# Optimization experiments

Hardware: AMD Instinct MI355X
Metric: run time of the kernel (lower is better)

Reference implementation:

```python
import jax, jax.numpy as jnp
import numpy as np


def ternarize_weight(w):
    # abs-mean threshold quantization to {-am, 0, +am}
    abs_mean = jnp.maximum(jnp.abs(w).mean(), 1e-5)
    thr = 0.7 * abs_mean
    q = jnp.where(w > thr, 1.0, jnp.where(w < -thr, -1.0, 0.0))
    # STE: forward value is q*abs_mean, grad flows to w as identity
    return w + jax.lax.stop_gradient(q * abs_mean - w)


def rotate_half(x):
    x1, x2 = jnp.split(x, 2, axis=-1)
    return jnp.concatenate([-x2, x1], axis=-1)


def setup_inputs() -> dict:
    key = jax.random.key(0)
    k1, k2, k3, k4, k5 = jax.random.split(key, 5)
    B, T, C, H = 2, 2048, 1024, 16
    D = C // H
    x = jax.random.normal(k1, (B, T, C), dtype=jnp.float32)
    cos = jax.random.uniform(k2, (1, 1, T, D), dtype=jnp.float32)
    sin = jax.random.uniform(k3, (1, 1, T, D), dtype=jnp.float32)
    w_qkv = jax.random.normal(k4, (3 * C, C), dtype=jnp.float32) / np.sqrt(C)
    w_proj = jax.random.normal(k5, (C, C), dtype=jnp.float32) / np.sqrt(C)
    return {"x": x, "cos": cos, "sin": sin, "w_qkv": w_qkv, "w_proj": w_proj}


def reference(x, cos, sin, w_qkv, w_proj):
    B, T, C = x.shape
    H = 16
    D = C // H
    wq = ternarize_weight(w_qkv)
    wp = ternarize_weight(w_proj)
    qkv = x @ wq.T  # [B,T,3C]
    q, k, v = jnp.split(qkv, 3, axis=-1)
    # [B,T,C] -> [B,H,T,D]
    q = q.reshape(B, T, H, D).transpose(0, 2, 1, 3)
    k = k.reshape(B, T, H, D).transpose(0, 2, 1, 3)
    v = v.reshape(B, T, H, D).transpose(0, 2, 1, 3)
    # RoPE
    q = q * cos + rotate_half(q) * sin
    k = k * cos + rotate_half(k) * sin
    # causal SDPA
    scale = 1.0 / np.sqrt(D)
    scores = jnp.einsum("bhqd,bhkd->bhqk", q, k) * scale
    causal = jnp.tril(jnp.ones((T, T), dtype=bool))
    scores = jnp.where(causal, scores, jnp.finfo(scores.dtype).min)
    attn = jax.nn.softmax(scores, axis=-1)
    y = jnp.einsum("bhqk,bhkd->bhqd", attn, v)  # [B,H,T,D]
    y = y.transpose(0, 2, 1, 3).reshape(B, T, C)
    return y @ wp.T
```

## Files before the change

### kernel.cpp

```cpp
#include <hip/hip_runtime.h>
#include <hip/hip_bf16.h>

#define B_ 2
#define T_ 2048
#define C_ 1024
#define H_ 16
#define D_ 64
#define M_ 4096
#define N3C 3072

using short8  = __attribute__((ext_vector_type(8))) short;
using floatx4 = __attribute__((ext_vector_type(4))) float;
typedef unsigned int u32;

__device__ __forceinline__ unsigned short f2b(float f) {
  __hip_bfloat16 h = __float2bfloat16(f);
  return *reinterpret_cast<unsigned short*>(&h);
}
__device__ __forceinline__ u32 pk2(float a, float b) {
  float2 t; t.x = a; t.y = b;
  __hip_bfloat162 p = __float22bfloat162_rn(t);
  return *reinterpret_cast<u32*>(&p);
}

#if __has_builtin(__builtin_amdgcn_exp2f)
__device__ __forceinline__ float ex2(float x) { return __builtin_amdgcn_exp2f(x); }
#else
__device__ __forceinline__ float ex2(float x) { return exp2f(x); }
#endif

__device__ __forceinline__ void gll16(const void* g, void* l) {
  __builtin_amdgcn_global_load_lds((const __attribute__((address_space(1))) u32*)g,
                                   (__attribute__((address_space(3))) u32*)l, 16, 0, 0);
}

#define SYNCV(N) do {                                                   \
    asm volatile("s_waitcnt vmcnt(" #N ")" ::: "memory");               \
    __builtin_amdgcn_s_barrier();                                       \
    asm volatile("" ::: "memory");                                      \
  } while (0)

__device__ __forceinline__ short8 xpnd(uint2 p) {
  u32 a = p.x, b = p.y;
  u32 d0 = ((a << 8) & 0x0000FF00u) | ((a << 16) & 0xFF000000u);
  u32 d1 = ((a >> 8) & 0x0000FF00u) | (a & 0xFF000000u);
  u32 d2 = ((b << 8) & 0x0000FF00u) | ((b << 16) & 0xFF000000u);
  u32 d3 = ((b >> 8) & 0x0000FF00u) | (b & 0xFF000000u);
  union { u32 d[4]; short8 s; } r;
  r.d[0] = d0; r.d[1] = d1; r.d[2] = d2; r.d[3] = d3;
  return r.s;
}


__global__ void abs_sum2(const float* __restrict__ wq, const float* __restrict__ wp,
                         double* __restrict__ sums) {
  __shared__ double red[4];
  const float* w = blockIdx.y ? wp : wq;
  const int n4 = blockIdx.y ? (C_ * C_ / 4) : (3 * C_ * C_ / 4);
  int stride = gridDim.x * blockDim.x;
  double s = 0.0;
  for (int i = blockIdx.x * blockDim.x + threadIdx.x; i < n4; i += stride) {
    float4 v = ((const float4*)w)[i];
    s += (double)fabsf(v.x) + (double)fabsf(v.y) + (double)fabsf(v.z) + (double)fabsf(v.w);
  }
  #pragma unroll
  for (int off = 32; off > 0; off >>= 1)
    s += __shfl_down(s, off, 64);
  if ((threadIdx.x & 63) == 0) red[threadIdx.x >> 6] = s;
  __syncthreads();
  if (threadIdx.x == 0) atomicAdd(sums + blockIdx.y, (red[0] + red[1]) + (red[2] + red[3]));
}

__global__ void tern_cvt(const float* __restrict__ wq, const float* __restrict__ wp,
                         const float* __restrict__ x,
                         unsigned char* __restrict__ oq, unsigned char* __restrict__ op,
                         unsigned short* __restrict__ xb,
                         const double* __restrict__ sums, float* __restrict__ ams) {
  const int NQ = 3 * C_ * C_;
  const int NP = C_ * C_;
  int i = blockIdx.x * blockDim.x + threadIdx.x;
  float am0 = fmaxf((float)(sums[0] * (1.0 / NQ)), 1e-5f);
  float am1 = fmaxf((float)(sums[1] * (1.0 / NP)), 1e-5f);
  if (i == 0) { ams[0] = am0; ams[1] = am1; }
  if (i < NQ) {
    float thr = 0.7f * am0, v = wq[i];
    oq[i] = (v > thr) ? 0x40u : ((v < -thr) ? 0xC0u : 0u);
  } else if (i < NQ + NP) {
    int j = i - NQ;
    float thr = 0.7f * am1, v = wp[j];
    op[j] = (v > thr) ? 0x40u : ((v < -thr) ? 0xC0u : 0u);
  } else {
    int j = i - NQ - NP;
    float4 v = ((const float4*)x)[j];
    ushort4 o; o.x = f2b(v.x); o.y = f2b(v.y); o.z = f2b(v.z); o.w = f2b(v.w);
    ((ushort4*)xb)[j] = o;
  }
}


__global__ __launch_bounds__(256) void gemm_qkv(const unsigned short* __restrict__ A,
                                                const unsigned char* __restrict__ W8,
                                                const float* __restrict__ scale_ptr,
                                                const float* __restrict__ cosp,
                                                const float* __restrict__ sinp,
                                                unsigned short* __restrict__ Qb,
                                                unsigned short* __restrict__ Kb,
                                                unsigned short* __restrict__ Vtb) {
  const int K = C_;
  __shared__ __attribute__((aligned(16))) unsigned short As[3][128 * 32];
  __shared__ __attribute__((aligned(16))) unsigned char  Ws[3][192 * 32];
  const int tid = threadIdx.x, lane = tid & 63, wv = tid >> 6;
  const int m = lane & 15, g = lane >> 4;
  const int m0 = blockIdx.y * 128, n0 = blockIdx.x * 192;
  const int wm = (wv >> 1) * 64, wn = wv & 1;
  const bool wlow = (wv < 2);

  const int srow16 = lane >> 2;
  const int skoff = (lane & 3) * 8;
  const unsigned short* ga0 = A + (size_t)(m0 + wv * 32 + srow16) * K + skoff;
  const unsigned short* ga1 = A + (size_t)(m0 + wv * 32 + 16 + srow16) * K + skoff;
  const unsigned char* gw0 = W8 + (size_t)(n0 + wv * 32 + (lane >> 1)) * K + (lane & 1) * 16;
  const unsigned char* gw1 = W8 + (size_t)(n0 + 128 + wv * 32 + (lane >> 1)) * K + (lane & 1) * 16;
  const int oA0 = (wv * 32) * 32;
  const int oA1 = (wv * 32 + 16) * 32;
  const int oW0 = (wv * 32) * 32;
  const int oW1 = ((128 + wv * 32)) * 32;

  floatx4 acc[4][6] = {};

#define QSTAGE(T) do {                                                    \
    gll16(ga0, &As[T][oA0]); gll16(ga1, &As[T][oA1]);                     \
    gll16(gw0, &Ws[T][oW0]);                                              \
    if (wlow) gll16(gw1, &Ws[T][oW1]);                                    \
    ga0 += 32; ga1 += 32; gw0 += 32; gw1 += 32;                           \
  } while (0)

#define QSYNC() do {                                                      \
    if (wlow) asm volatile("s_waitcnt vmcnt(4)" ::: "memory");            \
    else      asm volatile("s_waitcnt vmcnt(3)" ::: "memory");            \
    __builtin_amdgcn_s_barrier();                                         \
    asm volatile("" ::: "memory");                                        \
  } while (0)

#define QCOMP(T) do {                                                     \
    short8 af[4], wf[6];                                                  \
    _Pragma("unroll")                                                     \
    for (int r = 0; r < 4; r++)                                           \
      af[r] = *(const short8*)&As[T][(wm + r * 16 + m) * 32 + g * 8];     \
    _Pragma("unroll")                                                     \
    for (int j = 0; j < 6; j++)                                           \
      wf[j] = xpnd(*(const uint2*)&Ws[T][((2 * j + wn) * 16 + m) * 32 + g * 8]); \
    _Pragma("unroll")                                                     \
    for (int r = 0; r < 4; r++)                                           \
      _Pragma("unroll")                                                   \
      for (int j = 0; j < 6; j++)                                         \
        acc[r][j] = __builtin_amdgcn_mfma_f32_16x16x32_bf16(af[r], wf[j], acc[r][j], 0, 0, 0); \
  } while (0)

  QSTAGE(0);
  QSTAGE(1);
  QSYNC();
  for (int tt = 0; tt < 10; ++tt) {
    QSTAGE(2); QCOMP(0); QSYNC();
    QSTAGE(0); QCOMP(1); QSYNC();
    QSTAGE(1); QCOMP(2); QSYNC();
  }
  QCOMP(0); SYNCV(0);
  QCOMP(1);
#undef QSTAGE
#undef QSYNC
#undef QCOMP

  const float am = *scale_ptr;
  const float amh = am * 0.5f;
  #pragma unroll
  for (int j = 0; j < 6; j++) {
    const int colb = n0 + (2 * j + wn) * 16;
    const int sect = colb >> 10;
    const int h = (colb >> 6) & 15;
    const int pb = colb & 63;
    const int p = pb + m;
    if (sect < 2) {
      unsigned short* dst = sect ? Kb : Qb;
      const float sc = sect ? amh : amh * 0.18033688011112042f;
      const bool hi = (pb & 32) != 0;
      #pragma unroll
      for (int r = 0; r < 4; r++)
        #pragma unroll
        for (int i = 0; i < 4; i++) {
          int row = m0 + wm + r * 16 + g * 4 + i;
          int t = row & (T_ - 1), b = row >> 11;
          float cv = cosp[t * 64 + p], sv = sinp[t * 64 + p];
          float a = acc[r][j][i], pt = acc[r][j ^ 1][i];
          float val = hi ? (a * cv + pt * sv) : (a * cv - pt * sv);
          dst[((size_t)(b * H_ + h) * T_ + t) * 64 + p] = f2b(val * sc);
        }
    } else {
      #pragma unroll
      for (int r = 0; r < 4; r++)
        #pragma unroll
        for (int i = 0; i < 4; i++) {
          int row = m0 + wm + r * 16 + g * 4 + i;
          int t = row & (T_ - 1), b = row >> 11;
          size_t hbase = (size_t)(b * H_ + h) * 64 * T_;
          Vtb[hbase + (size_t)p * T_ + t] = f2b(acc[r][j][i] * amh);
        }
    }
  }
}


__global__ __launch_bounds__(256) void gemm_proj(const unsigned short* __restrict__ A,
                                                 const unsigned char* __restrict__ W8,
                                                 const float* __restrict__ scale_ptr,
                                                 float* __restrict__ Cout) {
  const int K = C_, N = C_;
  __shared__ __attribute__((aligned(16))) unsigned short As[3][128 * 32];
  __shared__ __attribute__((aligned(16))) unsigned char  Ws[3][128 * 32];
  const int tid = threadIdx.x, lane = tid & 63, wv = tid >> 6;
  const int m = lane & 15, g = lane >> 4;
  const int m0 = blockIdx.y * 128, n0 = blockIdx.x * 128;
  const int wm = (wv >> 1) * 64, wn = (wv & 1) * 64;

  const int srow16 = lane >> 2;
  const int skoff = (lane & 3) * 8;
  const unsigned short* ga0 = A + (size_t)(m0 + wv * 32 + srow16) * K + skoff;
  const unsigned short* ga1 = A + (size_t)(m0 + wv * 32 + 16 + srow16) * K + skoff;
  const unsigned char* gw0 = W8 + (size_t)(n0 + wv * 32 + (lane >> 1)) * K + (lane & 1) * 16;
  const int oA0 = (wv * 32) * 32;
  const int oA1 = (wv * 32 + 16) * 32;
  const int oW0 = (wv * 32) * 32;

  floatx4 acc[4][4] = {};

#define PSTAGE(T) do {                                                    \
    gll16(ga0, &As[T][oA0]); gll16(ga1, &As[T][oA1]);                     \
    gll16(gw0, &Ws[T][oW0]);                                              \
    ga0 += 32; ga1 += 32; gw0 += 32;                                      \
  } while (0)

#define PCOMP(T) do {                                                     \
    short8 af[4], wf[4];                                                  \
    _Pragma("unroll")                                                     \
    for (int r = 0; r < 4; r++)                                           \
      af[r] = *(const short8*)&As[T][(wm + r * 16 + m) * 32 + g * 8];     \
    _Pragma("unroll")                                                     \
    for (int c = 0; c < 4; c++)                                           \
      wf[c] = xpnd(*(const uint2*)&Ws[T][(wn + c * 16 + m) * 32 + g * 8]); \
    _Pragma("unroll")                                                     \
    for (int r = 0; r < 4; r++)                                           \
      _Pragma("unroll")                                                   \
      for (int c = 0; c < 4; c++)                                         \
        acc[r][c] = __builtin_amdgcn_mfma_f32_16x16x32_bf16(af[r], wf[c], acc[r][c], 0, 0, 0); \
  } while (0)

  PSTAGE(0);
  PSTAGE(1);
  SYNCV(3);
  for (int tt = 0; tt < 10; ++tt) {
    PSTAGE(2); PCOMP(0); SYNCV(3);
    PSTAGE(0); PCOMP(1); SYNCV(3);
    PSTAGE(1); PCOMP(2); SYNCV(3);
  }
  PCOMP(0); SYNCV(0);
  PCOMP(1);
#undef PSTAGE
#undef PCOMP

  const float scale = *scale_ptr * 0.5f;
  #pragma unroll
  for (int r = 0; r < 4; r++)
    #pragma unroll
    for (int c = 0; c < 4; c++)
      #pragma unroll
      for (int i = 0; i < 4; i++) {
        int row = m0 + wm + r * 16 + g * 4 + i;
        int col = n0 + wn + c * 16 + m;
        Cout[(size_t)row * N + col] = acc[r][c][i] * scale;
      }
}


__global__ __launch_bounds__(256) void flash_mfma(const unsigned short* __restrict__ Qb,
                                                  const unsigned short* __restrict__ Kb,
                                                  const unsigned short* __restrict__ Vtb,
                                                  unsigned short* __restrict__ Y) {
  __shared__ __align__(16) unsigned short Ktile[2][64][64];
  __shared__ __align__(16) unsigned short Vtile[2][64][64];
  __shared__ __align__(16) unsigned short Plds[4][16][72];
  const int lane = threadIdx.x & 63;
  const int wv = threadIdx.x >> 6;
  const int m = lane & 15, g = lane >> 4;
  const int gid = blockIdx.x;
  const int xcd = gid & 7, j = gid >> 3;
  const int bh = xcd * 4 + (j & 3);
  const int s = 31 - (j >> 2);
  const int b = bh >> 4, h = bh & 15;
  const size_t hb = (size_t)bh * T_ * 64;
  const unsigned short* Kbh = Kb + hb;
  const unsigned short* Vbh = Vtb + hb;
  const int r8 = lane >> 3, cc8 = lane & 7;
  const int gcol = ((cc8 ^ r8) << 3);

  const int ntiles = s + 1;
  const int qbase = s * 64 + wv * 16;
  const int q_glob = qbase + m;

  const unsigned short* qp = Qb + hb + (size_t)(qbase + m) * 64 + g * 8;
  short8 qf0 = *(const short8*)qp;
  short8 qf1 = *(const short8*)(qp + 32);

  short8 ones;
  #pragma unroll
  for (int i = 0; i < 8; i++) ones[i] = (short)0x3F80;

  floatx4 O[4] = {};
  floatx4 accl = {};

  #pragma unroll
  for (int cc = 0; cc < 2; cc++) {
    int row = wv * 16 + cc * 8;
    gll16(Kbh + (size_t)(row + r8) * 64 + gcol, &Ktile[0][row][0]);
    gll16(Vbh + (size_t)(row + r8) * T_ + gcol, &Vtile[0][row][0]);
  }

  for (int kt = 0; kt < ntiles; kt++) {
    const int buf = kt & 1;
    const int kb = kt * 64;
    __syncthreads();
    if (kt + 1 < ntiles) {
      const int kb2 = kb + 64;
      #pragma unroll
      for (int cc = 0; cc < 2; cc++) {
        int row = wv * 16 + cc * 8;
        gll16(Kbh + (size_t)(kb2 + row + r8) * 64 + gcol, &Ktile[1 - buf][row][0]);
        gll16(Vbh + (size_t)(row + r8) * T_ + kb2 + gcol, &Vtile[1 - buf][row][0]);
      }
    }
    floatx4 S[4];
    __builtin_amdgcn_s_setprio(1);
    #pragma unroll
    for (int mt = 0; mt < 4; mt++) {
      int row = mt * 16 + m;
      short8 kf0 = *(const short8*)&Ktile[buf][row][(g ^ (m & 7)) << 3];
      short8 kf1 = *(const short8*)&Ktile[buf][row][((g + 4) ^ (m & 7)) << 3];
      floatx4 sv = {};
      sv = __builtin_amdgcn_mfma_f32_16x16x32_bf16(kf0, qf0, sv, 0, 0, 0);
      sv = __builtin_amdgcn_mfma_f32_16x16x32_bf16(kf1, qf1, sv, 0, 0, 0);
      S[mt] = sv;
    }
    __builtin_amdgcn_s_setprio(0);
    if (kt + 1 < ntiles) {
      #pragma unroll
      for (int mt = 0; mt < 4; mt++) {
        uint2 w;
        w.x = pk2(ex2(S[mt][0]), ex2(S[mt][1]));
        w.y = pk2(ex2(S[mt][2]), ex2(S[mt][3]));
        *(uint2*)&Plds[wv][m][mt * 16 + g * 4] = w;
      }
    } else {
      #pragma unroll
      for (int mt = 0; mt < 4; mt++) {
        float e[4];
        #pragma unroll
        for (int r = 0; r < 4; r++) {
          int kg = kb + mt * 16 + g * 4 + r;
          e[r] = (kg <= q_glob) ? ex2(S[mt][r]) : 0.f;
        }
        uint2 w;
        w.x = pk2(e[0], e[1]);
        w.y = pk2(e[2], e[3]);
        *(uint2*)&Plds[wv][m][mt * 16 + g * 4] = w;
      }
    }
    short8 pa0 = *(const short8*)&Plds[wv][m][g * 8];
    short8 pa1 = *(const short8*)&Plds[wv][m][32 + g * 8];
    __builtin_amdgcn_s_setprio(1);
    #pragma unroll
    for (int nt = 0; nt < 4; nt++) {
      int row = nt * 16 + m;
      short8 v0 = *(const short8*)&Vtile[buf][row][(g ^ (m & 7)) << 3];
      short8 v1 = *(const short8*)&Vtile[buf][row][((g + 4) ^ (m & 7)) << 3];
      O[nt] = __builtin_amdgcn_mfma_f32_16x16x32_bf16(pa0, v0, O[nt], 0, 0, 0);
      O[nt] = __builtin_amdgcn_mfma_f32_16x16x32_bf16(pa1, v1, O[nt], 0, 0, 0);
    }
    accl = __builtin_amdgcn_mfma_f32_16x16x32_bf16(pa0, ones, accl, 0, 0, 0);
    accl = __builtin_amdgcn_mfma_f32_16x16x32_bf16(pa1, ones, accl, 0, 0, 0);
    __builtin_amdgcn_s_setprio(0);
  }

  float li[4];
  #pragma unroll
  for (int r = 0; r < 4; r++) li[r] = 1.0f / accl[r];
  #pragma unroll
  for (int nt = 0; nt < 4; nt++)
    #pragma unroll
    for (int r = 0; r < 4; r++) {
      int trow = qbase + g * 4 + r;
      int col = h * 64 + nt * 16 + m;
      Y[(size_t)(b * T_ + trow) * C_ + col] = f2b(O[nt][r] * li[r]);
    }
}


extern "C" void kernel_launch(void* const* d_in, const int* in_sizes, int n_in,
                              void* d_out, int out_size, void* d_ws, size_t ws_size,
                              hipStream_t stream) {
  (void)in_sizes; (void)n_in; (void)out_size; (void)ws_size;
  const float* x      = (const float*)d_in[0];
  const float* cosp   = (const float*)d_in[1];
  const float* sinp   = (const float*)d_in[2];
  const float* w_qkv  = (const float*)d_in[3];
  const float* w_proj = (const float*)d_in[4];
  float* out = (float*)d_out;

  char* ws = (char*)d_ws;
  double* sums = (double*)ws;
  float*  ams  = (float*)(ws + 16);
  unsigned char*  wqkv_b8  = (unsigned char*)(ws + 256);
  unsigned char*  wproj_b8 = wqkv_b8 + (size_t)N3C * C_;
  unsigned short* xb  = (unsigned short*)(wproj_b8 + (size_t)C_ * C_);
  unsigned short* Qb  = xb + (size_t)M_ * C_;
  unsigned short* Kb  = Qb + (size_t)B_ * H_ * T_ * D_;
  unsigned short* Vtb = Kb + (size_t)B_ * H_ * T_ * D_;
  unsigned short* yb  = Vtb + (size_t)B_ * H_ * T_ * D_;

  hipMemsetAsync(sums, 0, 16, stream);
  abs_sum2<<<dim3(256, 2), 256, 0, stream>>>(w_qkv, w_proj, sums);
  tern_cvt<<<(4 * C_ * C_ + M_ * C_ / 4) / 256, 256, 0, stream>>>(w_qkv, w_proj, x,
                                                                  wqkv_b8, wproj_b8, xb,
                                                                  sums, ams);
  gemm_qkv<<<dim3(N3C / 192, M_ / 128), 256, 0, stream>>>(xb, wqkv_b8, ams + 0,
                                                          cosp, sinp, Qb, Kb, Vtb);
  flash_mfma<<<1024, 256, 0, stream>>>(Qb, Kb, Vtb, yb);
  gemm_proj<<<dim3(C_ / 128, M_ / 128), 256, 0, stream>>>(yb, wproj_b8, ams + 1, out);
}
```

Before: 196.2 us.

## Process 128 query rows per flash block with two 16-row groups per wave

Each flash-attention block now covers 128 queries instead of 64, and each wave handles two 16-row query groups, so every K/V tile loaded into LDS is reused by twice as many queries. The grid is halved to 512 blocks. Waves whose queries end before the current tile skip the compute for that tile. In exchange, register pressure rises from the doubled accumulators, there are fewer blocks to hide latency, and waves within a block become imbalanced near the diagonal.

```diff
diff --git a/kernel.cpp b/kernel.cpp
--- a/kernel.cpp
+++ b/kernel.cpp
@@ -287,14 +287,14 @@
                                                   unsigned short* __restrict__ Y) {
   __shared__ __align__(16) unsigned short Ktile[2][64][64];
   __shared__ __align__(16) unsigned short Vtile[2][64][64];
-  __shared__ __align__(16) unsigned short Plds[4][16][72];
+  __shared__ __align__(16) unsigned short Plds[4][2][16][72];
   const int lane = threadIdx.x & 63;
   const int wv = threadIdx.x >> 6;
   const int m = lane & 15, g = lane >> 4;
   const int gid = blockIdx.x;
   const int xcd = gid & 7, j = gid >> 3;
   const int bh = xcd * 4 + (j & 3);
-  const int s = 31 - (j >> 2);
+  const int qb = 15 - (j >> 2);
   const int b = bh >> 4, h = bh & 15;
   const size_t hb = (size_t)bh * T_ * 64;
   const unsigned short* Kbh = Kb + hb;
@@ -302,20 +302,24 @@
   const int r8 = lane >> 3, cc8 = lane & 7;
   const int gcol = ((cc8 ^ r8) << 3);
 
-  const int ntiles = s + 1;
-  const int qbase = s * 64 + wv * 16;
-  const int q_glob = qbase + m;
-
-  const unsigned short* qp = Qb + hb + (size_t)(qbase + m) * 64 + g * 8;
-  short8 qf0 = *(const short8*)qp;
-  short8 qf1 = *(const short8*)(qp + 32);
+  const int ntiles = 2 * qb + 2;
+  const int q0 = qb * 128 + wv * 32;
+  const int t_d = q0 >> 6;
+
+  short8 qf[2][2];
+  #pragma unroll
+  for (int qg = 0; qg < 2; qg++) {
+    const unsigned short* qp = Qb + hb + (size_t)(q0 + qg * 16 + m) * 64 + g * 8;
+    qf[qg][0] = *(const short8*)qp;
+    qf[qg][1] = *(const short8*)(qp + 32);
+  }
 
   short8 ones;
   #pragma unroll
   for (int i = 0; i < 8; i++) ones[i] = (short)0x3F80;
 
-  floatx4 O[4] = {};
-  floatx4 accl = {};
+  floatx4 O[2][4] = {};
+  floatx4 accl[2] = {};
 
   #pragma unroll
   for (int cc = 0; cc < 2; cc++) {
@@ -337,69 +341,93 @@
         gll16(Vbh + (size_t)(row + r8) * T_ + kb2 + gcol, &Vtile[1 - buf][row][0]);
       }
     }
-    floatx4 S[4];
-    __builtin_amdgcn_s_setprio(1);
+    if (kt <= t_d) {
+      floatx4 S[2][4];
+      __builtin_amdgcn_s_setprio(1);
+      #pragma unroll
+      for (int mt = 0; mt < 4; mt++) {
+        int row = mt * 16 + m;
+        short8 kf0 = *(const short8*)&Ktile[buf][row][(g ^ (m & 7)) << 3];
+        short8 kf1 = *(const short8*)&Ktile[buf][row][((g + 4) ^ (m & 7)) << 3];
+        #pragma unroll
+        for (int qg = 0; qg < 2; qg++) {
+          floatx4 sv = (qg == 0) ? __builtin_amdgcn_mfma_f32_16x16x32_bf16(kf0, qf[0][0], floatx4{}, 0, 0, 0)
+                                 : __builtin_amdgcn_mfma_f32_16x16x32_bf16(kf0, qf[1][0], floatx4{}, 0, 0, 0);
+          sv = __builtin_amdgcn_mfma_f32_16x16x32_bf16(kf1, qf[qg][1], sv, 0, 0, 0);
+          S[qg][mt] = sv;
+        }
+      }
+      __builtin_amdgcn_s_setprio(0);
+      if (kt < t_d) {
+        #pragma unroll
+        for (int qg = 0; qg < 2; qg++)
+          #pragma unroll
+          for (int mt = 0; mt < 4; mt++) {
+            uint2 w;
+            w.x = pk2(ex2(S[qg][mt][0]), ex2(S[qg][mt][1]));
+            w.y = pk2(ex2(S[qg][mt][2]), ex2(S[qg][mt][3]));
+            *(uint2*)&Plds[wv][qg][m][mt * 16 + g * 4] = w;
+          }
+      } else {
+        #pragma unroll
+        for (int qg = 0; qg < 2; qg++) {
+          const int qglob = q0 + qg * 16 + m;
+          #pragma unroll
+          for (int mt = 0; mt < 4; mt++) {
+            float e[4];
+            #pragma unroll
+            for (int r = 0; r < 4; r++) {
+              int kg = kb + mt * 16 + g * 4 + r;
+              e[r] = (kg <= qglob) ? ex2(S[qg][mt][r]) : 0.f;
+            }
+            uint2 w;
+            w.x = pk2(e[0], e[1]);
+            w.y = pk2(e[2], e[3]);
+            *(uint2*)&Plds[wv][qg][m][mt * 16 + g * 4] = w;
+          }
+        }
+      }
+      short8 pa[2][2];
+      #pragma unroll
+      for (int qg = 0; qg < 2; qg++) {
+        pa[qg][0] = *(const short8*)&Plds[wv][qg][m][g * 8];
+        pa[qg][1] = *(const short8*)&Plds[wv][qg][m][32 + g * 8];
+      }
+      __builtin_amdgcn_s_setprio(1);
+      #pragma unroll
+      for (int nt = 0; nt < 4; nt++) {
+        int row = nt * 16 + m;
+        short8 v0 = *(const short8*)&Vtile[buf][row][(g ^ (m & 7)) << 3];
+        short8 v1 = *(const short8*)&Vtile[buf][row][((g + 4) ^ (m & 7)) << 3];
+        #pragma unroll
+        for (int qg = 0; qg < 2; qg++) {
+          O[qg][nt] = __builtin_amdgcn_mfma_f32_16x16x32_bf16(pa[qg][0], v0, O[qg][nt], 0, 0, 0);
+          O[qg][nt] = __builtin_amdgcn_mfma_f32_16x16x32_bf16(pa[qg][1], v1, O[qg][nt], 0, 0, 0);
+        }
+      }
+      #pragma unroll
+      for (int qg = 0; qg < 2; qg++) {
+        accl[qg] = __builtin_amdgcn_mfma_f32_16x16x32_bf16(pa[qg][0], ones, accl[qg], 0, 0, 0);
+        accl[qg] = __builtin_amdgcn_mfma_f32_16x16x32_bf16(pa[qg][1], ones, accl[qg], 0, 0, 0);
+      }
+      __builtin_amdgcn_s_setprio(0);
+    }
+  }
+
+  #pragma unroll
+  for (int qg = 0; qg < 2; qg++) {
+    float li[4];
     #pragma unroll
-    for (int mt = 0; mt < 4; mt++) {
-      int row = mt * 16 + m;
-      short8 kf0 = *(const short8*)&Ktile[buf][row][(g ^ (m & 7)) << 3];
-      short8 kf1 = *(const short8*)&Ktile[buf][row][((g + 4) ^ (m & 7)) << 3];
-      floatx4 sv = {};
-      sv = __builtin_amdgcn_mfma_f32_16x16x32_bf16(kf0, qf0, sv, 0, 0, 0);
-      sv = __builtin_amdgcn_mfma_f32_16x16x32_bf16(kf1, qf1, sv, 0, 0, 0);
-      S[mt] = sv;
-    }
-    __builtin_amdgcn_s_setprio(0);
-    if (kt + 1 < ntiles) {
-      #pragma unroll
-      for (int mt = 0; mt < 4; mt++) {
-        uint2 w;
-        w.x = pk2(ex2(S[mt][0]), ex2(S[mt][1]));
-        w.y = pk2(ex2(S[mt][2]), ex2(S[mt][3]));
-        *(uint2*)&Plds[wv][m][mt * 16 + g * 4] = w;
-      }
-    } else {
-      #pragma unroll
-      for (int mt = 0; mt < 4; mt++) {
-        float e[4];
-        #pragma unroll
-        for (int r = 0; r < 4; r++) {
-          int kg = kb + mt * 16 + g * 4 + r;
-          e[r] = (kg <= q_glob) ? ex2(S[mt][r]) : 0.f;
-        }
-        uint2 w;
-        w.x = pk2(e[0], e[1]);
-        w.y = pk2(e[2], e[3]);
-        *(uint2*)&Plds[wv][m][mt * 16 + g * 4] = w;
-      }
-    }
-    short8 pa0 = *(const short8*)&Plds[wv][m][g * 8];
-    short8 pa1 = *(const short8*)&Plds[wv][m][32 + g * 8];
-    __builtin_amdgcn_s_setprio(1);
+    for (int r = 0; r < 4; r++) li[r] = 1.0f / accl[qg][r];
     #pragma unroll
-    for (int nt = 0; nt < 4; nt++) {
-      int row = nt * 16 + m;
-      short8 v0 = *(const short8*)&Vtile[buf][row][(g ^ (m & 7)) << 3];
-      short8 v1 = *(const short8*)&Vtile[buf][row][((g + 4) ^ (m & 7)) << 3];
-      O[nt] = __builtin_amdgcn_mfma_f32_16x16x32_bf16(pa0, v0, O[nt], 0, 0, 0);
-      O[nt] = __builtin_amdgcn_mfma_f32_16x16x32_bf16(pa1, v1, O[nt], 0, 0, 0);
-    }
-    accl = __builtin_amdgcn_mfma_f32_16x16x32_bf16(pa0, ones, accl, 0, 0, 0);
-    accl = __builtin_amdgcn_mfma_f32_16x16x32_bf16(pa1, ones, accl, 0, 0, 0);
-    __builtin_amdgcn_s_setprio(0);
-  }
-
-  float li[4];
-  #pragma unroll
-  for (int r = 0; r < 4; r++) li[r] = 1.0f / accl[r];
-  #pragma unroll
-  for (int nt = 0; nt < 4; nt++)
-    #pragma unroll
-    for (int r = 0; r < 4; r++) {
-      int trow = qbase + g * 4 + r;
-      int col = h * 64 + nt * 16 + m;
-      Y[(size_t)(b * T_ + trow) * C_ + col] = f2b(O[nt][r] * li[r]);
-    }
+    for (int nt = 0; nt < 4; nt++)
+      #pragma unroll
+      for (int r = 0; r < 4; r++) {
+        int trow = q0 + qg * 16 + g * 4 + r;
+        int col = h * 64 + nt * 16 + m;
+        Y[(size_t)(b * T_ + trow) * C_ + col] = f2b(O[qg][nt][r] * li[r]);
+      }
+  }
 }
 
 
@@ -432,6 +460,6 @@
                                                                   sums, ams);
   gemm_qkv<<<dim3(N3C / 192, M_ / 128), 256, 0, stream>>>(xb, wqkv_b8, ams + 0,
                                                           cosp, sinp, Qb, Kb, Vtb);
-  flash_mfma<<<1024, 256, 0, stream>>>(Qb, Kb, Vtb, yb);
+  flash_mfma<<<512, 256, 0, stream>>>(Qb, Kb, Vtb, yb);
   gemm_proj<<<dim3(C_ / 128, M_ / 128), 256, 0, stream>>>(yb, wproj_b8, ams + 1, out);
 }
```

After: 208.0 us. 6.0% more time.
